# Kernel tuning notes

Measured on AMD Instinct MI355X. Metric: run time of the kernel, lower is better.

## Reference

```python
import jax, jax.numpy as jnp
import numpy as np

P = 1024
D_FF = 4096
TGT = 4096
SRC = 4096


def _ln(x, g, b, eps=1e-5):
    mu = jnp.mean(x, axis=-1, keepdims=True)
    var = jnp.mean((x - mu) ** 2, axis=-1, keepdims=True)
    return (x - mu) / jnp.sqrt(var + eps) * g + b


def setup_inputs() -> dict:
    key = jax.random.key(0)
    ks = jax.random.split(key, 32)
    s = 1.0 / np.sqrt(P)
    sf = 1.0 / np.sqrt(D_FF)
    d = {
        "Y": jax.random.normal(ks[0], (TGT, P), jnp.float32),
        "Xp": jax.random.normal(ks[1], (SRC, P), jnp.float32),
        # self-attn projections (Linear: y = x @ W + b, W stored [in, out])
        "wq1": jax.random.uniform(ks[2], (P, P), jnp.float32, -s, s),
        "bq1": jnp.zeros((P,), jnp.float32),
        "wk1": jax.random.uniform(ks[3], (P, P), jnp.float32, -s, s),
        "bk1": jnp.zeros((P,), jnp.float32),
        "wv1": jax.random.uniform(ks[4], (P, P), jnp.float32, -s, s),
        "bv1": jnp.zeros((P,), jnp.float32),
        "w0": jax.random.uniform(ks[5], (P, P), jnp.float32, -s, s),
        "b0": jnp.zeros((P,), jnp.float32),
        "g1": jnp.ones((P,), jnp.float32),
        "be1": jnp.zeros((P,), jnp.float32),
        # cross-attn projections
        "wq2": jax.random.uniform(ks[6], (P, P), jnp.float32, -s, s),
        "bq2": jnp.zeros((P,), jnp.float32),
        "wk2": jax.random.uniform(ks[7], (P, P), jnp.float32, -s, s),
        "bk2": jnp.zeros((P,), jnp.float32),
        "wv2": jax.random.uniform(ks[8], (P, P), jnp.float32, -s, s),
        "bv2": jnp.zeros((P,), jnp.float32),
        "w1": jax.random.uniform(ks[9], (P, P), jnp.float32, -s, s),
        "b1": jnp.zeros((P,), jnp.float32),
        "g2": jnp.ones((P,), jnp.float32),
        "be2": jnp.zeros((P,), jnp.float32),
        # FFN
        "w2": jax.random.uniform(ks[10], (P, D_FF), jnp.float32, -s, s),
        "b2": jnp.zeros((D_FF,), jnp.float32),
        "w3": jax.random.uniform(ks[11], (D_FF, P), jnp.float32, -sf, sf),
        "b3": jnp.zeros((P,), jnp.float32),
        "g3": jnp.ones((P,), jnp.float32),
        "be3": jnp.zeros((P,), jnp.float32),
    }
    return d


def reference(Y, Xp, wq1, bq1, wk1, bk1, wv1, bv1, w0, b0, g1, be1,
              wq2, bq2, wk2, bk2, wv2, bv2, w1, b1, g2, be2,
              w2, b2, w3, b3, g3, be3):
    m = Y.shape[0]
    scale = 1.0 / jnp.sqrt(jnp.asarray(P, Y.dtype))
    # --- masked self-attention on Y ---
    Q = Y @ wq1 + bq1            # [m, p]
    K = Y @ wk1 + bk1
    V = Y @ wv1 + bv1
    S = (Q @ K.T) * scale        # [m, m]
    causal = jnp.tril(jnp.ones((m, m), bool))
    S = jnp.where(causal, S, jnp.asarray(-1e9, S.dtype))
    A = jax.nn.softmax(S, axis=-1)
    T1 = (A @ V) @ w0 + b0
    U1 = _ln(Y + T1, g1, be1)
    # --- cross-attention with encoder output Xp ---
    Q = U1 @ wq2 + bq2           # [m, p]
    K = Xp @ wk2 + bk2           # [n, p]
    V = Xp @ wv2 + bv2
    S = (Q @ K.T) * scale        # [m, n]
    A = jax.nn.softmax(S, axis=-1)
    T2 = (A @ V) @ w1 + b1
    U2 = _ln(U1 + T2, g2, be2)
    # --- position-wise FFN ---
    Z = jax.nn.relu(U2 @ w2 + b2) @ w3 + b3
    U3 = _ln(U2 + Z, g3, be3)
    return U3
```

## Files before the change

kernel.cpp:

```cpp
#include <hip/hip_runtime.h>
#include <hip/hip_bf16.h>

typedef __bf16 bf16x8 __attribute__((ext_vector_type(8)));
typedef __bf16 bf16x4 __attribute__((ext_vector_type(4)));
typedef float f32x4 __attribute__((ext_vector_type(4)));

#define AS1P(p) ((__attribute__((address_space(1))) void*)(void*)(p))
#define AS3P(p) ((__attribute__((address_space(3))) void*)(p))

__global__ __launch_bounds__(256, 3) void gemm_bt(
    const __hip_bfloat16* __restrict__ A, int lda,
    const __hip_bfloat16* __restrict__ Bt, int ldb,
    int M, int N, int K, int ldc,
    const float* __restrict__ bias, int bias_mode,
    float scale,
    const float* __restrict__ residual,
    int relu, int causal_skip, int trapezoid, int ksplit,
    float* __restrict__ Cf, __hip_bfloat16* __restrict__ Cb,
    int nsplit1, const __hip_bfloat16* __restrict__ A2,
    const __hip_bfloat16* __restrict__ Bt2, int ldb2, int ldc2,
    const float* __restrict__ bias2, __hip_bfloat16* __restrict__ Cb2)
{
    int nb = blockIdx.x;
    int mb = blockIdx.y;
    {
        const int gx = gridDim.x, gy = gridDim.y;
        if ((gx & 3) == 0 && (gy & 1) == 0) {
            const int id = mb * gx + nb;
            const int X  = id & 7;
            const int L  = id >> 3;
            const int rn = gx >> 2, rm = gy >> 1;
            const int nb_l = L / rm, mb_l = L - nb_l * rm;
            nb = (X & 3) * rn + nb_l;
            mb = (X >> 2) * rm + mb_l;
        }
    }
    if (nsplit1 && nb >= nsplit1) {
        A = A2; Bt = Bt2; ldb = ldb2; ldc = ldc2; bias = bias2;
        Cb = Cb2; Cf = nullptr; residual = nullptr;
        nb -= nsplit1;
    }
    const int m_base = mb * 128;
    const int n_base = nb * 128;
    if (causal_skip && (n_base > m_base + 127)) return;
    int Kend = K;
    if (trapezoid) { int kl = m_base + 128; Kend = kl < K ? kl : K; }
    int kb = 0, ke = Kend;
    if (ksplit) {
        kb = blockIdx.z * ksplit;
        int k2 = kb + ksplit; ke = k2 < Kend ? k2 : Kend;
        if (kb >= ke) return;
        Cb += (size_t)blockIdx.z * M * ldc;
        Cf = nullptr;
    }
    const int nt = (ke - kb) >> 5;

    __shared__ __align__(16) __hip_bfloat16 Lds[3][8192];

    const int tid  = threadIdx.x;
    const int lane = tid & 63;
    const int wave = tid >> 6;
    const int wm = (wave >> 1) * 64;
    const int wn = (wave & 1) * 64;

    f32x4 acc[4][4];
#pragma unroll
    for (int i = 0; i < 4; ++i)
#pragma unroll
        for (int j = 0; j < 4; ++j) acc[i][j] = f32x4{0.f, 0.f, 0.f, 0.f};

    const bool isA = wave < 2;
    const __hip_bfloat16* G = isA ? (A + (size_t)m_base * lda) : (Bt + (size_t)n_base * ldb);
    const int ldg = isA ? lda : ldb;
    const int q0 = (wave & 1) * 4;
    const int rsub = lane >> 2;
    const int cx   = (lane & 3) ^ ((lane >> 3) & 3);
    const size_t grow = (size_t)(q0 * 16 + rsub) * ldg + (size_t)cx * 8 + kb;
    const int ldsoff = (isA ? 0 : 4096) + q0 * 512;

    const int lrow = lane & 15;
    const int cph  = ((lane >> 4) ^ ((lrow >> 1) & 3)) * 8;

#define ISSUE_TILE(KT, STG)                                                      \
    {                                                                            \
        const __hip_bfloat16* g = G + grow + (size_t)(KT) * 32;                  \
        __hip_bfloat16* dst = &Lds[STG][ldsoff];                                 \
        _Pragma("unroll")                                                        \
        for (int q = 0; q < 4; ++q) {                                            \
            __builtin_amdgcn_global_load_lds(AS1P(g), AS3P(dst), 16, 0, 0);      \
            g += (size_t)16 * ldg; dst += 512;                                   \
        }                                                                        \
    }

    ISSUE_TILE(0, 0)
    if (nt > 1) ISSUE_TILE(1, 1)

    int cur = 0;
    for (int kt = 0; kt < nt; ++kt) {
        __builtin_amdgcn_sched_barrier(0);
        if (kt + 1 < nt) __builtin_amdgcn_s_waitcnt(0x0F74);
        else             __builtin_amdgcn_s_waitcnt(0x0F70);
        __builtin_amdgcn_sched_barrier(0);
        __builtin_amdgcn_s_barrier();
        __builtin_amdgcn_sched_barrier(0);
        if (kt + 2 < nt) {
            int s2 = cur + 2; if (s2 >= 3) s2 -= 3;
            ISSUE_TILE(kt + 2, s2)
        }

        bf16x8 af[4], bfv[4];
#pragma unroll
        for (int i = 0; i < 4; ++i)
            af[i] = *(const bf16x8*)&Lds[cur][(wm + i * 16 + lrow) * 32 + cph];
#pragma unroll
        for (int j = 0; j < 4; ++j)
            bfv[j] = *(const bf16x8*)&Lds[cur][4096 + (wn + j * 16 + lrow) * 32 + cph];
#pragma unroll
        for (int i = 0; i < 4; ++i)
#pragma unroll
            for (int j = 0; j < 4; ++j)
                acc[i][j] = __builtin_amdgcn_mfma_f32_16x16x32_bf16(af[i], bfv[j], acc[i][j], 0, 0, 0);

        cur = (cur + 1 == 3) ? 0 : cur + 1;
    }
#undef ISSUE_TILE

    const int r0 = (lane >> 4) * 4;
    const int c0 = lane & 15;
#pragma unroll
    for (int i = 0; i < 4; ++i) {
#pragma unroll
        for (int j = 0; j < 4; ++j) {
            const int col = n_base + wn + j * 16 + c0;
#pragma unroll
            for (int r = 0; r < 4; ++r) {
                const int row = m_base + wm + i * 16 + r0 + r;
                float v = acc[i][j][r] * scale;
                if (bias_mode == 1) v += bias[col];
                else if (bias_mode == 2) v += bias[row];
                if (relu) v = fmaxf(v, 0.f);
                const size_t idx = (size_t)row * ldc + col;
                if (residual) v += residual[idx];
                if (Cf) Cf[idx] = v;
                else    Cb[idx] = __float2bfloat16(v);
            }
        }
    }
}

__global__ __launch_bounds__(256, 2) void gemm_bt2(
    const __hip_bfloat16* __restrict__ A, int lda,
    const __hip_bfloat16* __restrict__ Bt, int ldb,
    int M, int N, int K, int ldc,
    const float* __restrict__ bias, int bias_mode,
    float scale,
    int relu, int causal_skip, int trapezoid, int ksplit,
    __hip_bfloat16* __restrict__ Cb,
    int nsplit1, const __hip_bfloat16* __restrict__ A2,
    const __hip_bfloat16* __restrict__ Bt2, int ldb2, int ldc2,
    const float* __restrict__ bias2, __hip_bfloat16* __restrict__ Cb2)
{
    int nb = blockIdx.x;
    int mb = blockIdx.y;
    {
        const int gx = gridDim.x, gy = gridDim.y;
        if ((gx & 3) == 0 && (gy & 1) == 0) {
            const int id = mb * gx + nb;
            const int X  = id & 7;
            const int L  = id >> 3;
            const int rn = gx >> 2, rm = gy >> 1;
            const int nb_l = L / rm, mb_l = L - nb_l * rm;
            nb = (X & 3) * rn + nb_l;
            mb = (X >> 2) * rm + mb_l;
        }
    }
    if (nsplit1 && nb >= nsplit1) {
        A = A2; Bt = Bt2; ldb = ldb2; ldc = ldc2; bias = bias2;
        Cb = Cb2;
        nb -= nsplit1;
    }
    const int m_base = mb * 256;
    const int n_base = nb * 128;
    if (causal_skip && (n_base > m_base + 255)) return;
    int Kend = K;
    if (trapezoid) { int kl = m_base + 256; Kend = kl < K ? kl : K; }
    int kb = 0, ke = Kend;
    if (ksplit) {
        kb = blockIdx.z * ksplit;
        int k2 = kb + ksplit; ke = k2 < Kend ? k2 : Kend;
        if (kb >= ke) return;
        Cb += (size_t)blockIdx.z * M * ldc;
    }
    const int nt = (ke - kb) >> 5;

    __shared__ __align__(16) __hip_bfloat16 Lds[3][12288];

    const int tid  = threadIdx.x;
    const int lane = tid & 63;
    const int wave = tid >> 6;
    const int wtm = (wave >> 1) * 128;
    const int wtn = (wave & 1) * 64;

    f32x4 acc[8][4];
#pragma unroll
    for (int i = 0; i < 8; ++i)
#pragma unroll
        for (int j = 0; j < 4; ++j) acc[i][j] = f32x4{0.f, 0.f, 0.f, 0.f};

    const int rsub = lane >> 2;
    const int cx   = (lane & 3) ^ ((lane >> 3) & 3);
    const __hip_bfloat16* GA = A  + (size_t)(m_base + wave * 64) * lda + (size_t)rsub * lda + (size_t)cx * 8 + kb;
    const __hip_bfloat16* GB = Bt + (size_t)(n_base + wave * 32) * ldb + (size_t)rsub * ldb + (size_t)cx * 8 + kb;
    const int ldsA = wave * 2048;
    const int ldsB = 8192 + wave * 1024;

    const int lrow = lane & 15;
    const int cph  = ((lane >> 4) ^ ((lrow >> 1) & 3)) * 8;

#define ISSUE_TILE2(KT, STG)                                                     \
    {                                                                            \
        const size_t ko = (size_t)(KT) * 32;                                     \
        const __hip_bfloat16* ga = GA + ko;                                      \
        __hip_bfloat16* da = &Lds[STG][ldsA];                                    \
        _Pragma("unroll")                                                        \
        for (int q = 0; q < 4; ++q) {                                            \
            __builtin_amdgcn_global_load_lds(AS1P(ga), AS3P(da), 16, 0, 0);      \
            ga += (size_t)16 * lda; da += 512;                                   \
        }                                                                        \
        const __hip_bfloat16* gb = GB + ko;                                      \
        __hip_bfloat16* db = &Lds[STG][ldsB];                                    \
        _Pragma("unroll")                                                        \
        for (int q = 0; q < 2; ++q) {                                            \
            __builtin_amdgcn_global_load_lds(AS1P(gb), AS3P(db), 16, 0, 0);      \
            gb += (size_t)16 * ldb; db += 512;                                   \
        }                                                                        \
    }

    ISSUE_TILE2(0, 0)
    if (nt > 1) ISSUE_TILE2(1, 1)

    int cur = 0;
    for (int kt = 0; kt < nt; ++kt) {
        __builtin_amdgcn_sched_barrier(0);
        if (kt + 1 < nt) __builtin_amdgcn_s_waitcnt(0x0F76);
        else             __builtin_amdgcn_s_waitcnt(0x0F70);
        __builtin_amdgcn_sched_barrier(0);
        __builtin_amdgcn_s_barrier();
        __builtin_amdgcn_sched_barrier(0);
        if (kt + 2 < nt) {
            int s2 = cur + 2; if (s2 >= 3) s2 -= 3;
            ISSUE_TILE2(kt + 2, s2)
        }

        bf16x8 af[8], bfv[4];
#pragma unroll
        for (int i = 0; i < 8; ++i)
            af[i] = *(const bf16x8*)&Lds[cur][(wtm + i * 16 + lrow) * 32 + cph];
#pragma unroll
        for (int j = 0; j < 4; ++j)
            bfv[j] = *(const bf16x8*)&Lds[cur][8192 + (wtn + j * 16 + lrow) * 32 + cph];
#pragma unroll
        for (int i = 0; i < 8; ++i)
#pragma unroll
            for (int j = 0; j < 4; ++j)
                acc[i][j] = __builtin_amdgcn_mfma_f32_16x16x32_bf16(af[i], bfv[j], acc[i][j], 0, 0, 0);

        cur = (cur + 1 == 3) ? 0 : cur + 1;
    }
#undef ISSUE_TILE2

    const int r0 = (lane >> 4) * 4;
    const int c0 = lane & 15;
#pragma unroll
    for (int i = 0; i < 8; ++i) {
#pragma unroll
        for (int j = 0; j < 4; ++j) {
            const int col = n_base + wtn + j * 16 + c0;
#pragma unroll
            for (int r = 0; r < 4; ++r) {
                const int row = m_base + wtm + i * 16 + r0 + r;
                float v = acc[i][j][r] * scale;
                if (bias_mode == 1) v += bias[col];
                else if (bias_mode == 2) v += bias[row];
                if (relu) v = fmaxf(v, 0.f);
                Cb[(size_t)row * ldc + col] = __float2bfloat16(v);
            }
        }
    }
}

__global__ __launch_bounds__(256) void reduce_k_kernel(
    const __hip_bfloat16* __restrict__ Pb, int M, int N, int nsplit, int KC, int trapK,
    const float* __restrict__ bias, const float* __restrict__ residual,
    float* __restrict__ Cf, __hip_bfloat16* __restrict__ Cb)
{
    const int idx = blockIdx.x * 256 + threadIdx.x;
    const int nv = N >> 2;
    const int row = idx / nv;
    if (row >= M) return;
    const int c4 = (idx - row * nv) * 4;
    int nc = nsplit;
    if (trapK) {
        int kend = (row & ~255) + 256; if (kend > trapK) kend = trapK;
        nc = (kend + KC - 1) / KC;
    }
    float s0 = 0.f, s1 = 0.f, s2 = 0.f, s3 = 0.f;
    for (int c = 0; c < nc; ++c) {
        const bf16x4 p = *(const bf16x4*)(Pb + ((size_t)c * M + row) * N + c4);
        s0 += (float)p[0]; s1 += (float)p[1]; s2 += (float)p[2]; s3 += (float)p[3];
    }
    if (bias) {
        const f32x4 b = *(const f32x4*)(bias + c4);
        s0 += b[0]; s1 += b[1]; s2 += b[2]; s3 += b[3];
    }
    if (residual) {
        const f32x4 rv = *(const f32x4*)(residual + (size_t)row * N + c4);
        s0 += rv[0]; s1 += rv[1]; s2 += rv[2]; s3 += rv[3];
    }
    if (Cf) { f32x4 o = {s0, s1, s2, s3}; *(f32x4*)(Cf + (size_t)row * N + c4) = o; }
    else {
        bf16x4 o = { (__bf16)s0, (__bf16)s1, (__bf16)s2, (__bf16)s3 };
        *(bf16x4*)(Cb + (size_t)row * N + c4) = o;
    }
}

__global__ __launch_bounds__(256) void reduce_ln_kernel(
    const __hip_bfloat16* __restrict__ Pb, int M, int nsplit,
    const float* __restrict__ bias, const float* __restrict__ residual,
    const float* __restrict__ g, const float* __restrict__ b,
    float* __restrict__ outF, __hip_bfloat16* __restrict__ outB)
{
    __shared__ float sm[8];
    const int row = blockIdx.x;
    const int tid = threadIdx.x;
    const int c4 = tid * 4;

    float v0 = 0.f, v1 = 0.f, v2 = 0.f, v3 = 0.f;
    for (int c = 0; c < nsplit; ++c) {
        const bf16x4 p = *(const bf16x4*)(Pb + ((size_t)c * M + row) * 1024 + c4);
        v0 += (float)p[0]; v1 += (float)p[1]; v2 += (float)p[2]; v3 += (float)p[3];
    }
    {
        const f32x4 bv = *(const f32x4*)(bias + c4);
        v0 += bv[0]; v1 += bv[1]; v2 += bv[2]; v3 += bv[3];
    }
    {
        const f32x4 rv = *(const f32x4*)(residual + (size_t)row * 1024 + c4);
        v0 += rv[0]; v1 += rv[1]; v2 += rv[2]; v3 += rv[3];
    }

    float s  = v0 + v1 + v2 + v3;
    float ss = v0 * v0 + v1 * v1 + v2 * v2 + v3 * v3;
#pragma unroll
    for (int o = 32; o; o >>= 1) { s += __shfl_down(s, o); ss += __shfl_down(ss, o); }
    if ((tid & 63) == 0) { sm[tid >> 6] = s; sm[4 + (tid >> 6)] = ss; }
    __syncthreads();
    s  = sm[0] + sm[1] + sm[2] + sm[3];
    ss = sm[4] + sm[5] + sm[6] + sm[7];
    const float mu   = s * (1.f / 1024.f);
    const float var  = ss * (1.f / 1024.f) - mu * mu;
    const float rstd = rsqrtf(var + 1e-5f);
    const float4 gv = ((const float4*)g)[tid];
    const float4 bv = ((const float4*)b)[tid];
    float4 o;
    o.x = (v0 - mu) * rstd * gv.x + bv.x;
    o.y = (v1 - mu) * rstd * gv.y + bv.y;
    o.z = (v2 - mu) * rstd * gv.z + bv.z;
    o.w = (v3 - mu) * rstd * gv.w + bv.w;
    ((float4*)(outF + (size_t)row * 1024))[tid] = o;
    if (outB) {
        bf16x4 ob = { (__bf16)o.x, (__bf16)o.y, (__bf16)o.z, (__bf16)o.w };
        *(bf16x4*)(outB + (size_t)row * 1024 + c4) = ob;
    }
}

__global__ __launch_bounds__(256) void convert_bf16_kernel(
    const float* __restrict__ x, __hip_bfloat16* __restrict__ y, int n4)
{
    const int i = blockIdx.x * 256 + threadIdx.x;
    if (i >= n4) return;
    const float4 v = ((const float4*)x)[i];
    bf16x4 o = { (__bf16)v.x, (__bf16)v.y, (__bf16)v.z, (__bf16)v.w };
    *(bf16x4*)(y + (size_t)i * 4) = o;
}

__global__ __launch_bounds__(256) void transpose_convert_kernel(
    const float* __restrict__ W, __hip_bfloat16* __restrict__ Wt, int K, int N)
{
    __shared__ float t[32][33];
    const int k0 = blockIdx.y * 32;
    const int n0 = blockIdx.x * 32;
    const int tx = threadIdx.x;
    for (int i = threadIdx.y; i < 32; i += 8)
        t[i][tx] = W[(size_t)(k0 + i) * N + n0 + tx];
    __syncthreads();
    for (int i = threadIdx.y; i < 32; i += 8)
        Wt[(size_t)(n0 + i) * K + k0 + tx] = __float2bfloat16(t[tx][i]);
}

__global__ __launch_bounds__(256) void transpose_bf16_kernel(
    const __hip_bfloat16* __restrict__ src, int ls,
    __hip_bfloat16* __restrict__ dst, int ld)
{
    __shared__ __hip_bfloat16 t[32][33];
    const int r0 = blockIdx.y * 32;
    const int c0 = blockIdx.x * 32;
    const int tx = threadIdx.x;
    for (int i = threadIdx.y; i < 32; i += 8)
        t[i][tx] = src[(size_t)(r0 + i) * ls + c0 + tx];
    __syncthreads();
    for (int i = threadIdx.y; i < 32; i += 8)
        dst[(size_t)(c0 + i) * ld + r0 + tx] = t[tx][i];
}

__global__ __launch_bounds__(256) void softmax_kernel(
    const __hip_bfloat16* __restrict__ S, __hip_bfloat16* __restrict__ A, int N, int causal)
{
    __shared__ float sm[4];
    const int row = blockIdx.x;
    const int tid = threadIdx.x;
    const int limit = causal ? (row + 1) : N;
    const int zl0 = (row & ~255) + 256;
    const int zlimit = causal ? (zl0 < N ? zl0 : N) : N;
    const __hip_bfloat16* Srow = S + (size_t)row * N;
    __hip_bfloat16* Arow = A + (size_t)row * N;

    float x[4][4];
    float m = -3.0e38f;
#pragma unroll
    for (int p = 0; p < 4; ++p) {
        const int cb = p * 1024 + tid * 4;
        if (cb < limit) {
            const bf16x4 xv = *(const bf16x4*)(Srow + cb);
#pragma unroll
            for (int e = 0; e < 4; ++e) {
                const float f = (cb + e < limit) ? (float)xv[e] : -3.0e38f;
                x[p][e] = f;
                m = fmaxf(m, f);
            }
        } else {
#pragma unroll
            for (int e = 0; e < 4; ++e) x[p][e] = -3.0e38f;
        }
    }
#pragma unroll
    for (int o = 32; o; o >>= 1) m = fmaxf(m, __shfl_down(m, o));
    if ((tid & 63) == 0) sm[tid >> 6] = m;
    __syncthreads();
    m = fmaxf(fmaxf(sm[0], sm[1]), fmaxf(sm[2], sm[3]));
    __syncthreads();

    float s = 0.f;
#pragma unroll
    for (int p = 0; p < 4; ++p) {
        const int cb = p * 1024 + tid * 4;
        if (cb < limit) {
#pragma unroll
            for (int e = 0; e < 4; ++e) {
                const float ev = (cb + e < limit) ? __expf(x[p][e] - m) : 0.f;
                x[p][e] = ev;
                s += ev;
            }
        } else {
#pragma unroll
            for (int e = 0; e < 4; ++e) x[p][e] = 0.f;
        }
    }
#pragma unroll
    for (int o = 32; o; o >>= 1) s += __shfl_down(s, o);
    if ((tid & 63) == 0) sm[tid >> 6] = s;
    __syncthreads();
    s = sm[0] + sm[1] + sm[2] + sm[3];
    const float inv = 1.f / s;

#pragma unroll
    for (int p = 0; p < 4; ++p) {
        const int cb = p * 1024 + tid * 4;
        if (cb < zlimit) {
            bf16x4 o = { (__bf16)(x[p][0] * inv), (__bf16)(x[p][1] * inv),
                         (__bf16)(x[p][2] * inv), (__bf16)(x[p][3] * inv) };
            *(bf16x4*)(Arow + cb) = o;
        }
    }
}

extern "C" void kernel_launch(void* const* d_in, const int* in_sizes, int n_in,
                              void* d_out, int out_size, void* d_ws, size_t ws_size,
                              hipStream_t stream)
{
    const int M = 4096, Pd = 1024, DFF = 4096, NS = 4096;
    const size_t MB = 1024 * 1024;

    const float* Y   = (const float*)d_in[0];
    const float* Xp  = (const float*)d_in[1];
    const float* wq1 = (const float*)d_in[2];  const float* bq1 = (const float*)d_in[3];
    const float* wk1 = (const float*)d_in[4];  const float* bk1 = (const float*)d_in[5];
    const float* wv1 = (const float*)d_in[6];  const float* bv1 = (const float*)d_in[7];
    const float* w0  = (const float*)d_in[8];  const float* b0  = (const float*)d_in[9];
    const float* g1  = (const float*)d_in[10]; const float* be1 = (const float*)d_in[11];
    const float* wq2 = (const float*)d_in[12]; const float* bq2 = (const float*)d_in[13];
    const float* wk2 = (const float*)d_in[14]; const float* bk2 = (const float*)d_in[15];
    const float* wv2 = (const float*)d_in[16]; const float* bv2 = (const float*)d_in[17];
    const float* w1  = (const float*)d_in[18]; const float* b1  = (const float*)d_in[19];
    const float* g2  = (const float*)d_in[20]; const float* be2 = (const float*)d_in[21];
    const float* w2  = (const float*)d_in[22]; const float* b2  = (const float*)d_in[23];
    const float* w3  = (const float*)d_in[24]; const float* b3  = (const float*)d_in[25];
    const float* g3  = (const float*)d_in[26]; const float* be3 = (const float*)d_in[27];

    char* ws = (char*)d_ws;
    __hip_bfloat16* Ybf   = (__hip_bfloat16*)(ws + 0 * MB);
    __hip_bfloat16* Ubf   = (__hip_bfloat16*)(ws + 0 * MB);
    __hip_bfloat16* Xpbf  = (__hip_bfloat16*)(ws + 8 * MB);
    __hip_bfloat16* AVbf  = (__hip_bfloat16*)(ws + 8 * MB);
    __hip_bfloat16* Qbf   = (__hip_bfloat16*)(ws + 8 * MB);
    __hip_bfloat16* wqkv1t= (__hip_bfloat16*)(ws + 16 * MB);
    __hip_bfloat16* w0t   = (__hip_bfloat16*)(ws + 22 * MB);
    __hip_bfloat16* wq2t  = (__hip_bfloat16*)(ws + 24 * MB);
    __hip_bfloat16* wkv2t = (__hip_bfloat16*)(ws + 26 * MB);
    __hip_bfloat16* w1t   = (__hip_bfloat16*)(ws + 30 * MB);
    __hip_bfloat16* w2t   = (__hip_bfloat16*)(ws + 32 * MB);
    __hip_bfloat16* w3t   = (__hip_bfloat16*)(ws + 40 * MB);
    float*          bqkv1 = (float*)(ws + 48 * MB);
    float*          bkv2  = (float*)(ws + 48 * MB + 512 * 1024);
    __hip_bfloat16* QKV1  = (__hip_bfloat16*)(ws + 49 * MB);
    __hip_bfloat16* KV2   = (__hip_bfloat16*)(ws + 73 * MB);
    __hip_bfloat16* Vt    = (__hip_bfloat16*)(ws + 89 * MB);
    __hip_bfloat16* Sb    = (__hip_bfloat16*)(ws + 97 * MB);
    __hip_bfloat16* Pb    = (__hip_bfloat16*)(ws + 97 * MB);
    __hip_bfloat16* Abf   = (__hip_bfloat16*)(ws + 161 * MB);
    float*          Uf    = (float*)(ws + 209 * MB);
    float*          Out   = (float*)d_out;
    if (ws_size < 225 * MB) return;

    auto cvt = [&](const float* src, __hip_bfloat16* dst, int n) {
        convert_bf16_kernel<<<dim3(n / 1024), dim3(256), 0, stream>>>(src, dst, n / 4);
    };
    auto tconv = [&](const float* W, __hip_bfloat16* Wt, int K, int N) {
        transpose_convert_kernel<<<dim3(N / 32, K / 32), dim3(32, 8), 0, stream>>>(W, Wt, K, N);
    };
    auto tbf = [&](const __hip_bfloat16* src, int ls, __hip_bfloat16* dst, int ld, int R, int C) {
        transpose_bf16_kernel<<<dim3(C / 32, R / 32), dim3(32, 8), 0, stream>>>(src, ls, dst, ld);
    };
    auto gemm = [&](const __hip_bfloat16* A, int lda, const __hip_bfloat16* Bt, int ldb,
                    int Mm, int Nn, int Kk, int ldc,
                    const float* bias, int bmode, float scale, const float* res,
                    int relu, int causal, int trap, int ksplit,
                    float* Cf, __hip_bfloat16* Cb) {
        const int nz = ksplit ? (Kk + ksplit - 1) / ksplit : 1;
        gemm_bt<<<dim3(Nn / 128, Mm / 128, nz), dim3(256), 0, stream>>>(
            A, lda, Bt, ldb, Mm, Nn, Kk, ldc, bias, bmode, scale, res, relu, causal, trap, ksplit,
            Cf, Cb, 0, nullptr, nullptr, 0, 0, nullptr, nullptr);
    };
    auto gemm2 = [&](const __hip_bfloat16* A, int lda, const __hip_bfloat16* Bt, int ldb,
                     int Mm, int Nn, int Kk, int ldc,
                     const float* bias, int bmode, float scale,
                     int relu, int causal, int trap, int ksplit, __hip_bfloat16* Cb) {
        const int nz = ksplit ? (Kk + ksplit - 1) / ksplit : 1;
        gemm_bt2<<<dim3(Nn / 128, Mm / 256, nz), dim3(256), 0, stream>>>(
            A, lda, Bt, ldb, Mm, Nn, Kk, ldc, bias, bmode, scale, relu, causal, trap, ksplit, Cb,
            0, nullptr, nullptr, 0, 0, nullptr, nullptr);
    };
    auto reduce = [&](const __hip_bfloat16* P, int Mm, int Nn, int nsplit, int KC, int trapK,
                      const float* bias, const float* res, float* Cf, __hip_bfloat16* Cb) {
        reduce_k_kernel<<<dim3(Mm * Nn / 1024), dim3(256), 0, stream>>>(
            P, Mm, Nn, nsplit, KC, trapK, bias, res, Cf, Cb);
    };
    auto reduce_ln = [&](const __hip_bfloat16* P, int nsplit,
                         const float* bias, const float* res,
                         const float* gg, const float* bb,
                         float* outF, __hip_bfloat16* outB) {
        reduce_ln_kernel<<<dim3(M), dim3(256), 0, stream>>>(
            P, M, nsplit, bias, res, gg, bb, outF, outB);
    };

    const float scl = 0.03125f;

    cvt(Y,  Ybf,  M * Pd);
    cvt(Xp, Xpbf, NS * Pd);
    tconv(wq1, wqkv1t,            Pd, Pd);
    tconv(wk1, wqkv1t + Pd * Pd,  Pd, Pd);
    tconv(wv1, wqkv1t + 2*Pd*Pd,  Pd, Pd);
    tconv(w0,  w0t,  Pd, Pd);
    tconv(wq2, wq2t, Pd, Pd);
    tconv(wk2, wkv2t,           Pd, Pd);
    tconv(wv2, wkv2t + Pd * Pd, Pd, Pd);
    tconv(w1,  w1t,  Pd, Pd);
    tconv(w2, w2t, Pd, DFF);
    tconv(w3, w3t, DFF, Pd);
    hipMemcpyAsync(bqkv1,            bq1, Pd * 4, hipMemcpyDeviceToDevice, stream);
    hipMemcpyAsync(bqkv1 + Pd,       bk1, Pd * 4, hipMemcpyDeviceToDevice, stream);
    hipMemcpyAsync(bqkv1 + 2 * Pd,   bv1, Pd * 4, hipMemcpyDeviceToDevice, stream);
    hipMemcpyAsync(bkv2,             bk2, Pd * 4, hipMemcpyDeviceToDevice, stream);
    hipMemcpyAsync(bkv2 + Pd,        bv2, Pd * 4, hipMemcpyDeviceToDevice, stream);

    gemm_bt2<<<dim3(40, 16, 1), dim3(256), 0, stream>>>(
        Ybf, Pd, wqkv1t, Pd, M, 3072, Pd, 3072, bqkv1, 1, 1.f, 0, 0, 0, 0,
        QKV1,
        24, Xpbf, wkv2t, Pd, 2048, bkv2, KV2);

    tbf(QKV1 + 2048, 3072, Vt, M, M, Pd);
    gemm2(QKV1, 3072, QKV1 + 1024, 3072, M, M, Pd, M,
          nullptr, 0, scl, 0, 1, 0, 0, Sb);
    softmax_kernel<<<dim3(M), dim3(256), 0, stream>>>(Sb, Abf, M, 1);
    gemm2(Abf, M, Vt, M, M, Pd, M, Pd,
          nullptr, 0, 1.f, 0, 0, 1, 1024, Pb);
    reduce(Pb, M, Pd, 4, 1024, M, nullptr, nullptr, nullptr, AVbf);
    gemm(AVbf, Pd, w0t, Pd, M, Pd, Pd, Pd,
         nullptr, 0, 1.f, nullptr, 0, 0, 0, 512, nullptr, Pb);
    reduce_ln(Pb, 2, b0, Y, g1, be1, Uf, Ubf);

    gemm(Ubf, Pd, wq2t, Pd, M, Pd, Pd, Pd,
         nullptr, 0, 1.f, nullptr, 0, 0, 0, 512, nullptr, Pb);
    reduce(Pb, M, Pd, 2, 512, 0, bq2, nullptr, nullptr, Qbf);
    tbf(KV2 + 1024, 2048, Vt, NS, NS, Pd);
    gemm2(Qbf, Pd, KV2, 2048, M, NS, Pd, NS,
          nullptr, 0, scl, 0, 0, 0, 0, Sb);
    softmax_kernel<<<dim3(M), dim3(256), 0, stream>>>(Sb, Abf, NS, 0);
    gemm2(Abf, NS, Vt, NS, M, Pd, NS, Pd,
          nullptr, 0, 1.f, 0, 0, 0, 1024, Pb);
    reduce(Pb, M, Pd, 4, 1024, 0, nullptr, nullptr, nullptr, AVbf);
    gemm(AVbf, Pd, w1t, Pd, M, Pd, Pd, Pd,
         nullptr, 0, 1.f, nullptr, 0, 0, 0, 512, nullptr, Pb);
    reduce_ln(Pb, 2, b1, Uf, g2, be2, Uf, Ubf);

    gemm2(Ubf, Pd, w2t, Pd, M, DFF, Pd, DFF, b2, 1, 1.f, 1, 0, 0, 0, Abf);
    gemm2(Abf, DFF, w3t, DFF, M, Pd, DFF, Pd,
          nullptr, 0, 1.f, 0, 0, 0, 1024, Pb);
    reduce_ln(Pb, 4, b3, Uf, g3, be3, Out, nullptr);
}
```

Before: 742.4 us.

## Merge weight/input prep into one table-driven kernel and pack biases in a kernel

Replaces the ten per-weight transpose-convert launches and two fp32-to-bf16 convert launches with a single prep_kernel. It walks a block-offset table to pick the tensor for each block. The five device-to-device bias memcpys become one small bias_pack_kernel. The fused QKV1/KV2 projection moves from gemm_bt2 (256-row tiles) to gemm_bt (128-row tiles, more blocks), and gemm_bt2 loses its dual-problem split path. This cuts launch and memcpy overhead, but the non-transposed convert now uses scalar 32-wide accesses instead of float4 vectors.

```diff
diff --git a/kernel.cpp b/kernel.cpp
--- a/kernel.cpp
+++ b/kernel.cpp
@@ -155,10 +155,7 @@
     const float* __restrict__ bias, int bias_mode,
     float scale,
     int relu, int causal_skip, int trapezoid, int ksplit,
-    __hip_bfloat16* __restrict__ Cb,
-    int nsplit1, const __hip_bfloat16* __restrict__ A2,
-    const __hip_bfloat16* __restrict__ Bt2, int ldb2, int ldc2,
-    const float* __restrict__ bias2, __hip_bfloat16* __restrict__ Cb2)
+    __hip_bfloat16* __restrict__ Cb)
 {
     int nb = blockIdx.x;
     int mb = blockIdx.y;
@@ -173,11 +170,6 @@
             nb = (X & 3) * rn + nb_l;
             mb = (X >> 2) * rm + mb_l;
         }
-    }
-    if (nsplit1 && nb >= nsplit1) {
-        A = A2; Bt = Bt2; ldb = ldb2; ldc = ldc2; bias = bias2;
-        Cb = Cb2;
-        nb -= nsplit1;
     }
     const int m_base = mb * 256;
     const int n_base = nb * 128;
@@ -374,28 +366,57 @@
     }
 }
 
-__global__ __launch_bounds__(256) void convert_bf16_kernel(
-    const float* __restrict__ x, __hip_bfloat16* __restrict__ y, int n4)
+struct PrepTab {
+    const float* src[12];
+    __hip_bfloat16* dst[12];
+    int K[12];
+    int N[12];
+    int trans[12];
+    int blk0[13];
+};
+
+__global__ __launch_bounds__(256) void prep_kernel(PrepTab t)
+{
+    __shared__ float tile[32][33];
+    const int bid = blockIdx.x;
+    int e = 0;
+    while (e < 11 && bid >= t.blk0[e + 1]) ++e;
+    const int local = bid - t.blk0[e];
+    const int N = t.N[e];
+    const int K = t.K[e];
+    const int ntx = N >> 5;
+    const int n0 = (local % ntx) * 32;
+    const int k0 = (local / ntx) * 32;
+    const float* __restrict__ W = t.src[e];
+    __hip_bfloat16* __restrict__ D = t.dst[e];
+    const int tx = threadIdx.x;
+    const int ty = threadIdx.y;
+    if (t.trans[e]) {
+        for (int i = ty; i < 32; i += 8)
+            tile[i][tx] = W[(size_t)(k0 + i) * N + n0 + tx];
+        __syncthreads();
+        for (int i = ty; i < 32; i += 8)
+            D[(size_t)(n0 + i) * K + k0 + tx] = __float2bfloat16(tile[tx][i]);
+    } else {
+        for (int i = ty; i < 32; i += 8) {
+            const size_t idx = (size_t)(k0 + i) * N + n0 + tx;
+            D[idx] = __float2bfloat16(W[idx]);
+        }
+    }
+}
+
+__global__ __launch_bounds__(256) void bias_pack_kernel(
+    const float* __restrict__ bq1, const float* __restrict__ bk1,
+    const float* __restrict__ bv1, const float* __restrict__ bk2,
+    const float* __restrict__ bv2, float* __restrict__ bqkv1,
+    float* __restrict__ bkv2)
 {
     const int i = blockIdx.x * 256 + threadIdx.x;
-    if (i >= n4) return;
-    const float4 v = ((const float4*)x)[i];
-    bf16x4 o = { (__bf16)v.x, (__bf16)v.y, (__bf16)v.z, (__bf16)v.w };
-    *(bf16x4*)(y + (size_t)i * 4) = o;
-}
-
-__global__ __launch_bounds__(256) void transpose_convert_kernel(
-    const float* __restrict__ W, __hip_bfloat16* __restrict__ Wt, int K, int N)
-{
-    __shared__ float t[32][33];
-    const int k0 = blockIdx.y * 32;
-    const int n0 = blockIdx.x * 32;
-    const int tx = threadIdx.x;
-    for (int i = threadIdx.y; i < 32; i += 8)
-        t[i][tx] = W[(size_t)(k0 + i) * N + n0 + tx];
-    __syncthreads();
-    for (int i = threadIdx.y; i < 32; i += 8)
-        Wt[(size_t)(n0 + i) * K + k0 + tx] = __float2bfloat16(t[tx][i]);
+    if (i < 1024)       bqkv1[i] = bq1[i];
+    else if (i < 2048)  bqkv1[i] = bk1[i - 1024];
+    else if (i < 3072)  bqkv1[i] = bv1[i - 2048];
+    else if (i < 4096)  bkv2[i - 3072] = bk2[i - 3072];
+    else if (i < 5120)  bkv2[i - 3072] = bv2[i - 4096];
 }
 
 __global__ __launch_bounds__(256) void transpose_bf16_kernel(
@@ -532,12 +553,6 @@
     float*          Out   = (float*)d_out;
     if (ws_size < 225 * MB) return;
 
-    auto cvt = [&](const float* src, __hip_bfloat16* dst, int n) {
-        convert_bf16_kernel<<<dim3(n / 1024), dim3(256), 0, stream>>>(src, dst, n / 4);
-    };
-    auto tconv = [&](const float* W, __hip_bfloat16* Wt, int K, int N) {
-        transpose_convert_kernel<<<dim3(N / 32, K / 32), dim3(32, 8), 0, stream>>>(W, Wt, K, N);
-    };
     auto tbf = [&](const __hip_bfloat16* src, int ls, __hip_bfloat16* dst, int ld, int R, int C) {
         transpose_bf16_kernel<<<dim3(C / 32, R / 32), dim3(32, 8), 0, stream>>>(src, ls, dst, ld);
     };
@@ -557,8 +572,7 @@
                      int relu, int causal, int trap, int ksplit, __hip_bfloat16* Cb) {
         const int nz = ksplit ? (Kk + ksplit - 1) / ksplit : 1;
         gemm_bt2<<<dim3(Nn / 128, Mm / 256, nz), dim3(256), 0, stream>>>(
-            A, lda, Bt, ldb, Mm, Nn, Kk, ldc, bias, bmode, scale, relu, causal, trap, ksplit, Cb,
-            0, nullptr, nullptr, 0, 0, nullptr, nullptr);
+            A, lda, Bt, ldb, Mm, Nn, Kk, ldc, bias, bmode, scale, relu, causal, trap, ksplit, Cb);
     };
     auto reduce = [&](const __hip_bfloat16* P, int Mm, int Nn, int nsplit, int KC, int trapK,
                       const float* bias, const float* res, float* Cf, __hip_bfloat16* Cb) {
@@ -575,27 +589,30 @@
 
     const float scl = 0.03125f;
 
-    cvt(Y,  Ybf,  M * Pd);
-    cvt(Xp, Xpbf, NS * Pd);
-    tconv(wq1, wqkv1t,            Pd, Pd);
-    tconv(wk1, wqkv1t + Pd * Pd,  Pd, Pd);
-    tconv(wv1, wqkv1t + 2*Pd*Pd,  Pd, Pd);
-    tconv(w0,  w0t,  Pd, Pd);
-    tconv(wq2, wq2t, Pd, Pd);
-    tconv(wk2, wkv2t,           Pd, Pd);
-    tconv(wv2, wkv2t + Pd * Pd, Pd, Pd);
-    tconv(w1,  w1t,  Pd, Pd);
-    tconv(w2, w2t, Pd, DFF);
-    tconv(w3, w3t, DFF, Pd);
-    hipMemcpyAsync(bqkv1,            bq1, Pd * 4, hipMemcpyDeviceToDevice, stream);
-    hipMemcpyAsync(bqkv1 + Pd,       bk1, Pd * 4, hipMemcpyDeviceToDevice, stream);
-    hipMemcpyAsync(bqkv1 + 2 * Pd,   bv1, Pd * 4, hipMemcpyDeviceToDevice, stream);
-    hipMemcpyAsync(bkv2,             bk2, Pd * 4, hipMemcpyDeviceToDevice, stream);
-    hipMemcpyAsync(bkv2 + Pd,        bv2, Pd * 4, hipMemcpyDeviceToDevice, stream);
-
-    gemm_bt2<<<dim3(40, 16, 1), dim3(256), 0, stream>>>(
-        Ybf, Pd, wqkv1t, Pd, M, 3072, Pd, 3072, bqkv1, 1, 1.f, 0, 0, 0, 0,
-        QKV1,
+    {
+        PrepTab t;
+        const float* srcs[12]  = { wq1, wk1, wv1, w0, wq2, wk2, wv2, w1, w2, w3, Y, Xp };
+        __hip_bfloat16* dsts[12] = { wqkv1t, wqkv1t + Pd * Pd, wqkv1t + 2 * Pd * Pd,
+                                     w0t, wq2t, wkv2t, wkv2t + Pd * Pd, w1t,
+                                     w2t, w3t, Ybf, Xpbf };
+        const int Ks[12] = { Pd, Pd, Pd, Pd, Pd, Pd, Pd, Pd, Pd,  DFF, M,  NS };
+        const int Ns[12] = { Pd, Pd, Pd, Pd, Pd, Pd, Pd, Pd, DFF, Pd,  Pd, Pd };
+        const int trs[12] = { 1, 1, 1, 1, 1, 1, 1, 1, 1, 1, 0, 0 };
+        int acc = 0;
+        for (int e = 0; e < 12; ++e) {
+            t.src[e] = srcs[e]; t.dst[e] = dsts[e];
+            t.K[e] = Ks[e]; t.N[e] = Ns[e]; t.trans[e] = trs[e];
+            t.blk0[e] = acc;
+            acc += (Ns[e] / 32) * (Ks[e] / 32);
+        }
+        t.blk0[12] = acc;
+        prep_kernel<<<dim3(acc), dim3(32, 8), 0, stream>>>(t);
+    }
+    bias_pack_kernel<<<dim3(20), dim3(256), 0, stream>>>(bq1, bk1, bv1, bk2, bv2, bqkv1, bkv2);
+
+    gemm_bt<<<dim3(40, 32, 1), dim3(256), 0, stream>>>(
+        Ybf, Pd, wqkv1t, Pd, M, 3072, Pd, 3072, bqkv1, 1, 1.f, nullptr, 0, 0, 0, 0,
+        nullptr, QKV1,
         24, Xpbf, wkv2t, Pd, 2048, bkv2, KV2);
 
     tbf(QKV1 + 2048, 3072, Vt, M, M, Pd);
```

Measured after the change: 698.9 us. 1.06x faster.
